# Kernel tuning notes

Measured on AMD Instinct MI355X. Metric: run time of the kernel, lower is better.

## Reference

```python
import jax, jax.numpy as jnp
import numpy as np
from jax import lax


def conv3d(x, w, b):
    # x: [B,C,H,W,D], w: [O,I,kh,kw,kd], SAME padding (matches padding=k//2 for odd k)
    out = lax.conv_general_dilated(
        x, w, window_strides=(1, 1, 1), padding='SAME',
        dimension_numbers=('NCDHW', 'OIDHW', 'NCDHW'))
    return out + b[None, :, None, None, None]


def setup_inputs() -> dict:
    key = jax.random.key(0)
    ks = jax.random.split(key, 9)
    B, C, H, W, D = 2, 64, 16, 16, 16
    P = 64  # pab_channels
    s = 0.05
    return {
        'x': jax.random.normal(ks[0], (B, C, H, W, D), jnp.float32),
        'top_w': jax.random.normal(ks[1], (P, C, 1, 1, 1), jnp.float32) * s,
        'top_b': jax.random.normal(ks[2], (P,), jnp.float32) * s,
        'center_w': jax.random.normal(ks[3], (P, C, 1, 1, 1), jnp.float32) * s,
        'center_b': jax.random.normal(ks[4], (P,), jnp.float32) * s,
        'bottom_w': jax.random.normal(ks[5], (C, C, 3, 3, 3), jnp.float32) * s,
        'bottom_b': jax.random.normal(ks[6], (C,), jnp.float32) * s,
        'out_w': jax.random.normal(ks[7], (C, C, 3, 3, 3), jnp.float32) * s,
        'out_b': jax.random.normal(ks[8], (C,), jnp.float32) * s,
    }


def reference(x, top_w, top_b, center_w, center_b, bottom_w, bottom_b, out_w, out_b):
    B, C, H, W, D = x.shape
    N = H * W * D
    x_top = conv3d(x, top_w, top_b).reshape(B, -1, N)            # [B,P,N]
    x_center = conv3d(x, center_w, center_b).reshape(B, -1, N)   # [B,P,N]
    x_bottom = conv3d(x, bottom_w, bottom_b).reshape(B, C, N)    # [B,C,N]
    # sp_map[b,n,m] = sum_p center[b,p,n] * top[b,p,m]
    sp = jnp.einsum('bpn,bpm->bnm', x_center, x_top)             # [B,N,N]
    # GLOBAL softmax over the entire flattened NxN map per batch element
    sp = jax.nn.softmax(sp.reshape(B, N * N), axis=1).reshape(B, N, N)
    sp = jnp.einsum('bnm,bcm->bnc', sp, x_bottom)                # [B,N,C]
    # faithful to torch: plain reshape [B,N,C] -> [B,C,H,W,D] (no transpose)
    sp = sp.reshape(B, C, H, W, D)
    return conv3d(x + sp, out_w, out_b)
```

## Files before the change

### kernel.cpp

```cpp
#include <hip/hip_runtime.h>


typedef __attribute__((ext_vector_type(8))) short bf16x8;
typedef __attribute__((ext_vector_type(4))) short short4v;
typedef __attribute__((ext_vector_type(4))) float f32x4;

#define DEVI static __device__ __forceinline__

DEVI f32x4 MFMA16(bf16x8 a, bf16x8 b, f32x4 c) {
  return __builtin_amdgcn_mfma_f32_16x16x32_bf16(a, b, c, 0, 0, 0);
}
DEVI f32x4 zero4() { return (f32x4){0.f, 0.f, 0.f, 0.f}; }

DEVI unsigned short f2bf(float f) {
  unsigned u = __float_as_uint(f);
  return (unsigned short)((u + 0x7fffu + ((u >> 16) & 1u)) >> 16);
}
DEVI float bf2f(unsigned short u) { return __uint_as_float((unsigned)u << 16); }
DEVI float fexp2(float x) { return __builtin_amdgcn_exp2f(x); }

DEVI unsigned cvtpk(float lo, float hi) {
  unsigned d;
  asm("v_cvt_pk_bf16_f32 %0, %1, %2" : "=v"(d) : "v"(lo), "v"(hi));
  return d;
}
DEVI bf16x8 pack8(f32x4 a, f32x4 b) {
  union { unsigned u[4]; bf16x8 v; } r;
  r.u[0] = cvtpk(a[0], a[1]);
  r.u[1] = cvtpk(a[2], a[3]);
  r.u[2] = cvtpk(b[0], b[1]);
  r.u[3] = cvtpk(b[2], b[3]);
  return r.v;
}

DEVI void gll16(const unsigned short* g, unsigned short* l) {
  __builtin_amdgcn_global_load_lds(
      (const __attribute__((address_space(1))) void*)g,
      (__attribute__((address_space(3))) void*)l, 16, 0, 0);
}

DEVI int permM(int n) {
  return (n & ~63) | (n & 32) | ((n & 12) << 1) | ((n & 16) >> 2) | (n & 3);
}

__global__ void k_prep(const float* __restrict__ tw, const float* __restrict__ cw,
                       const float* __restrict__ bw, const float* __restrict__ ow,
                       const float* __restrict__ x,
                       unsigned short* __restrict__ wkTopF, unsigned short* __restrict__ wkCenF,
                       unsigned short* __restrict__ wkBotF, unsigned short* __restrict__ wkOutF,
                       unsigned short* __restrict__ xT, unsigned short* __restrict__ zbuf) {
  __shared__ float tile[64][65];
  int bx = blockIdx.x;
  int tid = threadIdx.x;
  if (bx == 0 && tid < 64) zbuf[tid] = 0;
  if (bx < 432) {
    int t = bx * 256 + tid;
    if (t < 4096) {
      int co = t >> 6, ci = t & 63;
      int cog = co >> 4, col = co & 15, kc = ci >> 5, kg = (ci & 31) >> 3, e = ci & 7;
      int dst = (((cog * 2 + kc) * 64) + col + 16 * kg) * 8 + e;
      wkTopF[dst] = f2bf(tw[t]);
      wkCenF[dst] = f2bf(cw[t]);
    }
    int k = t % 27;
    int ci = (t / 27) & 63;
    int co = t / (27 * 64);
    int cog = co >> 4, col = co & 15, kc = ci >> 5, kg = (ci & 31) >> 3, e = ci & 7;
    int dst = ((((cog * 27 + k) * 2 + kc) * 64) + col + 16 * kg) * 8 + e;
    wkBotF[dst] = f2bf(bw[t]);
    wkOutF[dst] = f2bf(ow[t]);
    return;
  }
  int bx2 = bx - 432;
  int b = bx2 >> 6;
  int n0 = (bx2 & 63) << 6;
  {
    int nl = tid & 63, cq = tid >> 6;
    const float* xb = x + (size_t)b * 262144;
#pragma unroll
    for (int j = 0; j < 16; j++) {
      int c = cq * 16 + j;
      tile[c][nl] = xb[(size_t)c * 4096 + n0 + nl];
    }
  }
  __syncthreads();
  {
    int n = tid >> 2, c0 = (tid & 3) << 4;
    bf16x8 o0, o1;
#pragma unroll
    for (int j = 0; j < 8; j++) {
      o0[j] = (short)f2bf(tile[c0 + j][n]);
      o1[j] = (short)f2bf(tile[c0 + 8 + j][n]);
    }
    unsigned short* dst = xT + ((size_t)(b * 4096 + n0 + n)) * 64 + c0;
    *(bf16x8*)(dst) = o0;
    *(bf16x8*)(dst + 8) = o1;
  }
}

template <int OMODE>
DEVI void conv3_body(int bx, int t,
                     const unsigned short* __restrict__ wkF,
                     const unsigned short* __restrict__ xTb,
                     const float* __restrict__ bias,
                     const unsigned short* __restrict__ zbuf,
                     float* __restrict__ outF, unsigned short* __restrict__ outH,
                     unsigned short* hl) {
  int ch = bx & 1, wp = (bx >> 1) & 7, h = (bx >> 4) & 15, b = bx >> 8;
  int lane = t & 63, w = t >> 6;
  int col = lane & 15, kg = lane >> 4;
  const unsigned short* xb = xTb + (size_t)b * 262144;
  int row8 = lane >> 3, blk = lane & 7;
#pragma unroll
  for (int q = 0; q < 6; q++) {
    int vi0 = w * 48 + q * 8;
    int vi = vi0 + row8;
    int dhv = vi >> 6, wv = (vi >> 4) & 3, dv = vi & 15;
    int hh = h + dhv - 1, ww = wp * 2 + wv - 1;
    bool val = ((unsigned)hh < 16u) & ((unsigned)ww < 16u);
    int sw = blk ^ (vi & 7);
    const unsigned short* src =
        val ? (xb + ((size_t)((hh * 256 + ww * 16 + dv)) << 6) + sw * 8) : (zbuf + blk * 8);
    gll16(src, hl + vi0 * 64);
  }
  __syncthreads();
  int wi = w >> 1;
  int cg = ch * 2 + (w & 1);
  const char* hlb = (const char*)hl;
  f32x4 acc0 = zero4(), acc1 = zero4();
#pragma unroll
  for (int k = 0; k < 27; k++) {
    const int dh = k / 9;
    const int dw = (k / 3) % 3;
    const int dz = k % 3 - 1;
    int dsum = col + dz;
    bool vd = (unsigned)dsum < 16u;
    int dcl = vd ? dsum : col;
    int sv = dh * 64 + (wi + dw) * 16 + dcl;
    const unsigned short* wfk = wkF + (((size_t)(cg * 27 + k)) << 10) + lane * 8;
#pragma unroll
    for (int kc = 0; kc < 2; kc++) {
      bf16x8 av = *(const bf16x8*)(wfk + (kc << 9));
      int g = (kc * 4 + kg) ^ (sv & 7);
      bf16x8 bv = *(const bf16x8*)(hlb + sv * 128 + g * 16);
      if (!vd) bv = (bf16x8){0, 0, 0, 0, 0, 0, 0, 0};
      if (kc == 0) acc0 = MFMA16(av, bv, acc0);
      else acc1 = MFMA16(av, bv, acc1);
    }
  }
  int n0c = h * 256 + (wp * 2 + wi) * 16 + col;
  int nst = (OMODE == 2) ? permM(n0c) : n0c;
#pragma unroll
  for (int r = 0; r < 4; r++) {
    int co = ch * 32 + (w & 1) * 16 + kg * 4 + r;
    float v = acc0[r] + acc1[r] + bias[co];
    if (OMODE == 2)
      outH[(size_t)(b * 64 + co) * 4096 + nst] = f2bf(v);
    else
      outF[(size_t)(b * 64 + co) * 4096 + nst] = v;
  }
}

__global__ __launch_bounds__(256, 2) void k_convA(
    const unsigned short* __restrict__ wkTf, const unsigned short* __restrict__ wkCf,
    const unsigned short* __restrict__ wkBf, const unsigned short* __restrict__ xTb,
    const float* __restrict__ tbias, const float* __restrict__ cbias,
    const float* __restrict__ bbias, const unsigned short* __restrict__ zbuf,
    unsigned short* __restrict__ topT, unsigned short* __restrict__ cenT,
    unsigned short* __restrict__ botS) {
  __shared__ __align__(16) unsigned short hl[192 * 64];
  int bx0 = blockIdx.x;
  int t = threadIdx.x;
  if (bx0 >= 512) {
    conv3_body<2>(bx0 - 512, t, wkBf, xTb, bbias, zbuf, nullptr, botS, hl);
    return;
  }
  int lane = t & 63, wid = t >> 6;
  int col = lane & 15, kg = lane >> 4;
  int bx = bx0;
  int b = bx >> 8;
  int rest = bx & 255;
  int nt = rest >> 1, ch = rest & 1;
  int cg = ch * 2 + (wid >> 1);
  int co0 = ch * 32 + (wid >> 1) * 16;
  int n0c = nt * 32 + (wid & 1) * 16 + col;
  const unsigned short* xb = xTb + (size_t)b * 262144;
  f32x4 aT0 = zero4(), aT1 = zero4(), aC0 = zero4(), aC1 = zero4();
#pragma unroll
  for (int kc = 0; kc < 2; kc++) {
    bf16x8 bv = *(const bf16x8*)(xb + (size_t)n0c * 64 + kc * 32 + kg * 8);
    bf16x8 avT = *(const bf16x8*)(wkTf + (((size_t)cg * 2 + kc) * 64 + lane) * 8);
    bf16x8 avC = *(const bf16x8*)(wkCf + (((size_t)cg * 2 + kc) * 64 + lane) * 8);
    if (kc == 0) {
      aT0 = MFMA16(avT, bv, aT0);
      aC0 = MFMA16(avC, bv, aC0);
    } else {
      aT1 = MFMA16(avT, bv, aT1);
      aC1 = MFMA16(avC, bv, aC1);
    }
  }
  const float LOG2E = 1.4426950408889634f;
  short4v sT, sC;
#pragma unroll
  for (int r = 0; r < 4; r++) {
    float bvT = tbias[co0 + kg * 4 + r];
    float bvC = cbias[co0 + kg * 4 + r];
    sT[r] = (short)f2bf(aT0[r] + aT1[r] + bvT);
    sC[r] = (short)f2bf((aC0[r] + aC1[r] + bvC) * LOG2E);
  }
  size_t o = (size_t)(b * 4096 + n0c) * 64 + co0 + kg * 4;
  *(short4v*)(topT + o) = sT;
  *(short4v*)(cenT + o) = sC;
}

__global__ __launch_bounds__(256, 2) void k_convOut(
    const unsigned short* __restrict__ wkOf, const unsigned short* __restrict__ xTb,
    const float* __restrict__ bias, const unsigned short* __restrict__ zbuf,
    float* __restrict__ outF) {
  __shared__ __align__(16) unsigned short hl[192 * 64];
  conv3_body<1>(blockIdx.x, threadIdx.x, wkOf, xTb, bias, zbuf, outF, nullptr, hl);
}

__global__ __launch_bounds__(256, 2) void k_pass2(
    const unsigned short* __restrict__ cenT, const unsigned short* __restrict__ topT,
    const unsigned short* __restrict__ botS,
    unsigned short* __restrict__ part, float* __restrict__ Zpart) {
  __shared__ __align__(16) unsigned short topS[2][4096];
  __shared__ __align__(16) unsigned short botL[2][4096];
  __shared__ float zred[4];
  int bx = blockIdx.x;
  int b = bx >> 8;
  int ntp = (bx >> 3) & 31;
  int mc = bx & 7;
  int t = threadIdx.x;
  int lane = t & 63, w = t >> 6;
  int col = lane & 15, kg = lane >> 4;
  const unsigned short* cb = cenT + (size_t)b * 262144;
  const unsigned short* tb = topT + (size_t)b * 262144;
  const unsigned short* bb = botS + (size_t)b * 262144;
  int nA = ntp * 128 + w * 16;
  int mcBase = mc * 512;
  int row8 = lane >> 3, blk = lane & 7;
  int sw = blk ^ (row8 & 7);

  bf16x8 aA0 = *(const bf16x8*)(cb + (size_t)(nA + col) * 64 + kg * 8);
  bf16x8 aA1 = *(const bf16x8*)(cb + (size_t)(nA + col) * 64 + 32 + kg * 8);
  bf16x8 aB0 = *(const bf16x8*)(cb + (size_t)(nA + 64 + col) * 64 + kg * 8);
  bf16x8 aB1 = *(const bf16x8*)(cb + (size_t)(nA + 64 + col) * 64 + 32 + kg * 8);

  if (w < 2) {
#pragma unroll
    for (int q = 0; q < 4; q++) {
      int s = w * 4 + q;
      gll16(tb + (size_t)(mcBase + s * 8 + row8) * 64 + sw * 8, &topS[0][s * 512]);
    }
  } else {
#pragma unroll
    for (int q = 0; q < 4; q++) {
      int s = (w - 2) * 4 + q;
      gll16(bb + (size_t)(s * 8 + row8) * 4096 + mcBase + sw * 8, &botL[0][s * 512]);
    }
  }
  __syncthreads();

  f32x4 accOA[4], accOB[4];
#pragma unroll
  for (int ct = 0; ct < 4; ct++) {
    accOA[ct] = zero4();
    accOB[ct] = zero4();
  }
  float zs = 0.f;
  int swc = (col & 7) << 3;

  for (int j = 0; j < 8; j++) {
    int cur = j & 1;
    if (j < 7) {
      int m0n = mcBase + (j + 1) * 64;
      if (w < 2) {
#pragma unroll
        for (int q = 0; q < 4; q++) {
          int s = w * 4 + q;
          gll16(tb + (size_t)(m0n + s * 8 + row8) * 64 + sw * 8, &topS[cur ^ 1][s * 512]);
        }
      } else {
#pragma unroll
        for (int q = 0; q < 4; q++) {
          int s = (w - 2) * 4 + q;
          gll16(bb + (size_t)(s * 8 + row8) * 4096 + m0n + sw * 8, &botL[cur ^ 1][s * 512]);
        }
      }
    }
    f32x4 sA[4], sB[4];
#pragma unroll
    for (int mt = 0; mt < 4; mt++) {
      bf16x8 b0 = *(const bf16x8*)&topS[cur][(mt * 16 + col) * 64 + ((kg * 8) ^ swc)];
      bf16x8 b1 = *(const bf16x8*)&topS[cur][(mt * 16 + col) * 64 + ((32 + kg * 8) ^ swc)];
      sA[mt] = MFMA16(b1, aA1, MFMA16(b0, aA0, zero4()));
      sB[mt] = MFMA16(b1, aB1, MFMA16(b0, aB0, zero4()));
    }
#pragma unroll
    for (int mt = 0; mt < 4; mt++)
#pragma unroll
      for (int r = 0; r < 4; r++) {
        sA[mt][r] = fexp2(sA[mt][r]);
        sB[mt][r] = fexp2(sB[mt][r]);
        zs += sA[mt][r] + sB[mt][r];
      }
#pragma unroll
    for (int kc = 0; kc < 2; kc++) {
      bf16x8 paA = pack8(sA[2 * kc], sA[2 * kc + 1]);
      bf16x8 paB = pack8(sB[2 * kc], sB[2 * kc + 1]);
#pragma unroll
      for (int ct = 0; ct < 4; ct++) {
        bf16x8 bv = *(const bf16x8*)&botL[cur][(ct * 16 + col) * 64 + ((kc * 32 + kg * 8) ^ swc)];
        accOA[ct] = MFMA16(paA, bv, accOA[ct]);
        accOB[ct] = MFMA16(paB, bv, accOB[ct]);
      }
    }
    __syncthreads();
  }
  unsigned short* po = part + (((size_t)(b * 8 + mc) * 4096 + nA) << 6);
#pragma unroll
  for (int ct = 0; ct < 4; ct++)
#pragma unroll
    for (int r = 0; r < 4; r++) {
      po[(kg * 4 + r) * 64 + ct * 16 + col] = f2bf(accOA[ct][r]);
      po[(64 + kg * 4 + r) * 64 + ct * 16 + col] = f2bf(accOB[ct][r]);
    }
#pragma unroll
  for (int off = 32; off; off >>= 1) zs += __shfl_xor(zs, off);
  if (lane == 0) zred[w] = zs;
  __syncthreads();
  if (t == 0) Zpart[b * 256 + ntp * 8 + mc] = zred[0] + zred[1] + zred[2] + zred[3];
}

__global__ void k_xt1(const float* __restrict__ x, const unsigned short* __restrict__ part,
                      const float* __restrict__ Zpart, unsigned short* __restrict__ xT) {
  __shared__ float tile[64][65];
  __shared__ float zr[4];
  int bx = blockIdx.x;
  int b = bx >> 6;
  int n0 = (bx & 63) << 6;
  int t = threadIdx.x;
  float zv = Zpart[b * 256 + t];
#pragma unroll
  for (int off = 32; off; off >>= 1) zv += __shfl_xor(zv, off);
  if ((t & 63) == 0) zr[t >> 6] = zv;
  __syncthreads();
  float invZ = 1.0f / (zr[0] + zr[1] + zr[2] + zr[3]);
  {
    int c = t >> 2, nl16 = (t & 3) << 4;
    int nt6 = n0 >> 6;
    float acc[16];
#pragma unroll
    for (int k = 0; k < 16; k++) acc[k] = 0.f;
#pragma unroll
    for (int mcq = 0; mcq < 8; mcq++) {
      const unsigned short* pp =
          part + (((size_t)(b * 8 + mcq) * 4096) + c * 64 + nt6) * 64 + nl16;
      bf16x8 v0 = *(const bf16x8*)pp;
      bf16x8 v1 = *(const bf16x8*)(pp + 8);
#pragma unroll
      for (int k = 0; k < 8; k++) {
        acc[k] += bf2f((unsigned short)v0[k]);
        acc[8 + k] += bf2f((unsigned short)v1[k]);
      }
    }
    const float* xb = x + (size_t)b * 262144 + (size_t)c * 4096 + n0 + nl16;
#pragma unroll
    for (int q = 0; q < 4; q++) {
      f32x4 xv = *(const f32x4*)(xb + q * 4);
#pragma unroll
      for (int k = 0; k < 4; k++) tile[c][nl16 + q * 4 + k] = xv[k] + acc[q * 4 + k] * invZ;
    }
  }
  __syncthreads();
  {
    int n = t >> 2, c0 = (t & 3) << 4;
    bf16x8 o0, o1;
#pragma unroll
    for (int j = 0; j < 8; j++) {
      o0[j] = (short)f2bf(tile[c0 + j][n]);
      o1[j] = (short)f2bf(tile[c0 + 8 + j][n]);
    }
    unsigned short* dst = xT + ((size_t)(b * 4096 + n0 + n)) * 64 + c0;
    *(bf16x8*)(dst) = o0;
    *(bf16x8*)(dst + 8) = o1;
  }
}

extern "C" void kernel_launch(void* const* d_in, const int* in_sizes, int n_in,
                              void* d_out, int out_size, void* d_ws, size_t ws_size,
                              hipStream_t stream) {
  const float* x = (const float*)d_in[0];
  const float* tw = (const float*)d_in[1];
  const float* tb = (const float*)d_in[2];
  const float* cw = (const float*)d_in[3];
  const float* cbb = (const float*)d_in[4];
  const float* bw = (const float*)d_in[5];
  const float* bb = (const float*)d_in[6];
  const float* ow = (const float*)d_in[7];
  const float* ob = (const float*)d_in[8];
  float* out = (float*)d_out;
  char* ws = (char*)d_ws;

  unsigned short* wkTopF = (unsigned short*)(ws + 0);
  unsigned short* wkCenF = (unsigned short*)(ws + 8192);
  unsigned short* wkBotF = (unsigned short*)(ws + 16384);
  unsigned short* wkOutF = (unsigned short*)(ws + 237568);
  unsigned short* xT = (unsigned short*)(ws + 458752);
  unsigned short* topT = (unsigned short*)(ws + 1507328);
  unsigned short* cenT = (unsigned short*)(ws + 2555904);
  unsigned short* botS = (unsigned short*)(ws + 3604480);
  unsigned short* yT = (unsigned short*)(ws + 4653056);
  unsigned short* part = (unsigned short*)(ws + 5701632);
  float* Zpart = (float*)(ws + 14090240);
  unsigned short* zbuf = (unsigned short*)(ws + 14092288);

  k_prep<<<560, 256, 0, stream>>>(tw, cw, bw, ow, x, wkTopF, wkCenF, wkBotF, wkOutF, xT, zbuf);
  k_convA<<<1024, 256, 0, stream>>>(wkTopF, wkCenF, wkBotF, xT, tb, cbb, bb, zbuf, topT, cenT, botS);
  k_pass2<<<512, 256, 0, stream>>>(cenT, topT, botS, part, Zpart);
  k_xt1<<<128, 256, 0, stream>>>(x, part, Zpart, yT);
  k_convOut<<<512, 256, 0, stream>>>(wkOutF, yT, ob, zbuf, out);
}
```

Baseline: 43.95 us.

## Regrid conv3 blocks to cover all channels and widen pass2 to 512 threads

After: 47.87 us. +8.9%, slower.

```diff
diff --git a/kernel.cpp b/kernel.cpp
--- a/kernel.cpp
+++ b/kernel.cpp
@@ -106,7 +106,7 @@
                      const unsigned short* __restrict__ zbuf,
                      float* __restrict__ outF, unsigned short* __restrict__ outH,
                      unsigned short* hl) {
-  int ch = bx & 1, wp = (bx >> 1) & 7, h = (bx >> 4) & 15, b = bx >> 8;
+  int b = bx >> 7, h = (bx >> 3) & 15, wp = bx & 7;
   int lane = t & 63, w = t >> 6;
   int col = lane & 15, kg = lane >> 4;
   const unsigned short* xb = xTb + (size_t)b * 262144;
@@ -124,8 +124,8 @@
     gll16(src, hl + vi0 * 64);
   }
   __syncthreads();
-  int wi = w >> 1;
-  int cg = ch * 2 + (w & 1);
+  int wi = w & 1;
+  int ch = w >> 1;
   const char* hlb = (const char*)hl;
   f32x4 acc0 = zero4(), acc1 = zero4();
 #pragma unroll
@@ -137,27 +137,32 @@
     bool vd = (unsigned)dsum < 16u;
     int dcl = vd ? dsum : col;
     int sv = dh * 64 + (wi + dw) * 16 + dcl;
-    const unsigned short* wfk = wkF + (((size_t)(cg * 27 + k)) << 10) + lane * 8;
+    const unsigned short* wf0 = wkF + (((size_t)((2 * ch) * 27 + k)) << 10) + lane * 8;
+    const unsigned short* wf1 = wkF + (((size_t)((2 * ch + 1) * 27 + k)) << 10) + lane * 8;
 #pragma unroll
     for (int kc = 0; kc < 2; kc++) {
-      bf16x8 av = *(const bf16x8*)(wfk + (kc << 9));
       int g = (kc * 4 + kg) ^ (sv & 7);
       bf16x8 bv = *(const bf16x8*)(hlb + sv * 128 + g * 16);
       if (!vd) bv = (bf16x8){0, 0, 0, 0, 0, 0, 0, 0};
-      if (kc == 0) acc0 = MFMA16(av, bv, acc0);
-      else acc1 = MFMA16(av, bv, acc1);
+      bf16x8 av0 = *(const bf16x8*)(wf0 + (kc << 9));
+      bf16x8 av1 = *(const bf16x8*)(wf1 + (kc << 9));
+      acc0 = MFMA16(av0, bv, acc0);
+      acc1 = MFMA16(av1, bv, acc1);
     }
   }
   int n0c = h * 256 + (wp * 2 + wi) * 16 + col;
   int nst = (OMODE == 2) ? permM(n0c) : n0c;
 #pragma unroll
-  for (int r = 0; r < 4; r++) {
-    int co = ch * 32 + (w & 1) * 16 + kg * 4 + r;
-    float v = acc0[r] + acc1[r] + bias[co];
-    if (OMODE == 2)
-      outH[(size_t)(b * 64 + co) * 4096 + nst] = f2bf(v);
-    else
-      outF[(size_t)(b * 64 + co) * 4096 + nst] = v;
+  for (int cgi = 0; cgi < 2; cgi++) {
+#pragma unroll
+    for (int r = 0; r < 4; r++) {
+      int co = (ch * 2 + cgi) * 16 + kg * 4 + r;
+      float v = (cgi ? acc1[r] : acc0[r]) + bias[co];
+      if (OMODE == 2)
+        outH[(size_t)(b * 64 + co) * 4096 + nst] = f2bf(v);
+      else
+        outF[(size_t)(b * 64 + co) * 4096 + nst] = v;
+    }
   }
 }
 
@@ -221,17 +226,17 @@
   conv3_body<1>(blockIdx.x, threadIdx.x, wkOf, xTb, bias, zbuf, outF, nullptr, hl);
 }
 
-__global__ __launch_bounds__(256, 2) void k_pass2(
+__global__ __launch_bounds__(512, 2) void k_pass2(
     const unsigned short* __restrict__ cenT, const unsigned short* __restrict__ topT,
     const unsigned short* __restrict__ botS,
     unsigned short* __restrict__ part, float* __restrict__ Zpart) {
   __shared__ __align__(16) unsigned short topS[2][4096];
   __shared__ __align__(16) unsigned short botL[2][4096];
-  __shared__ float zred[4];
+  __shared__ float zred[8];
   int bx = blockIdx.x;
-  int b = bx >> 8;
-  int ntp = (bx >> 3) & 31;
-  int mc = bx & 7;
+  int b = bx >> 7;
+  int ntp = (bx >> 2) & 31;
+  int mc = bx & 3;
   int t = threadIdx.x;
   int lane = t & 63, w = t >> 6;
   int col = lane & 15, kg = lane >> 4;
@@ -239,99 +244,93 @@
   const unsigned short* tb = topT + (size_t)b * 262144;
   const unsigned short* bb = botS + (size_t)b * 262144;
   int nA = ntp * 128 + w * 16;
-  int mcBase = mc * 512;
+  int mcBase = mc * 1024;
   int row8 = lane >> 3, blk = lane & 7;
   int sw = blk ^ (row8 & 7);
 
   bf16x8 aA0 = *(const bf16x8*)(cb + (size_t)(nA + col) * 64 + kg * 8);
   bf16x8 aA1 = *(const bf16x8*)(cb + (size_t)(nA + col) * 64 + 32 + kg * 8);
-  bf16x8 aB0 = *(const bf16x8*)(cb + (size_t)(nA + 64 + col) * 64 + kg * 8);
-  bf16x8 aB1 = *(const bf16x8*)(cb + (size_t)(nA + 64 + col) * 64 + 32 + kg * 8);
-
-  if (w < 2) {
-#pragma unroll
-    for (int q = 0; q < 4; q++) {
-      int s = w * 4 + q;
+
+  if (w < 4) {
+#pragma unroll
+    for (int q = 0; q < 2; q++) {
+      int s = w * 2 + q;
       gll16(tb + (size_t)(mcBase + s * 8 + row8) * 64 + sw * 8, &topS[0][s * 512]);
     }
   } else {
 #pragma unroll
-    for (int q = 0; q < 4; q++) {
-      int s = (w - 2) * 4 + q;
+    for (int q = 0; q < 2; q++) {
+      int s = (w - 4) * 2 + q;
       gll16(bb + (size_t)(s * 8 + row8) * 4096 + mcBase + sw * 8, &botL[0][s * 512]);
     }
   }
   __syncthreads();
 
-  f32x4 accOA[4], accOB[4];
-#pragma unroll
-  for (int ct = 0; ct < 4; ct++) {
-    accOA[ct] = zero4();
-    accOB[ct] = zero4();
-  }
+  f32x4 accO[4];
+#pragma unroll
+  for (int ct = 0; ct < 4; ct++) accO[ct] = zero4();
   float zs = 0.f;
   int swc = (col & 7) << 3;
 
-  for (int j = 0; j < 8; j++) {
+  for (int j = 0; j < 16; j++) {
     int cur = j & 1;
-    if (j < 7) {
+    if (j < 15) {
       int m0n = mcBase + (j + 1) * 64;
-      if (w < 2) {
-#pragma unroll
-        for (int q = 0; q < 4; q++) {
-          int s = w * 4 + q;
+      if (w < 4) {
+#pragma unroll
+        for (int q = 0; q < 2; q++) {
+          int s = w * 2 + q;
           gll16(tb + (size_t)(m0n + s * 8 + row8) * 64 + sw * 8, &topS[cur ^ 1][s * 512]);
         }
       } else {
 #pragma unroll
-        for (int q = 0; q < 4; q++) {
-          int s = (w - 2) * 4 + q;
+        for (int q = 0; q < 2; q++) {
+          int s = (w - 4) * 2 + q;
           gll16(bb + (size_t)(s * 8 + row8) * 4096 + m0n + sw * 8, &botL[cur ^ 1][s * 512]);
         }
       }
     }
-    f32x4 sA[4], sB[4];
+    f32x4 sA[4];
 #pragma unroll
     for (int mt = 0; mt < 4; mt++) {
       bf16x8 b0 = *(const bf16x8*)&topS[cur][(mt * 16 + col) * 64 + ((kg * 8) ^ swc)];
       bf16x8 b1 = *(const bf16x8*)&topS[cur][(mt * 16 + col) * 64 + ((32 + kg * 8) ^ swc)];
       sA[mt] = MFMA16(b1, aA1, MFMA16(b0, aA0, zero4()));
-      sB[mt] = MFMA16(b1, aB1, MFMA16(b0, aB0, zero4()));
     }
 #pragma unroll
     for (int mt = 0; mt < 4; mt++)
 #pragma unroll
       for (int r = 0; r < 4; r++) {
         sA[mt][r] = fexp2(sA[mt][r]);
-        sB[mt][r] = fexp2(sB[mt][r]);
-        zs += sA[mt][r] + sB[mt][r];
+        zs += sA[mt][r];
       }
 #pragma unroll
     for (int kc = 0; kc < 2; kc++) {
-      bf16x8 paA = pack8(sA[2 * kc], sA[2 * kc + 1]);
-      bf16x8 paB = pack8(sB[2 * kc], sB[2 * kc + 1]);
+      bf16x8 pa = pack8(sA[2 * kc], sA[2 * kc + 1]);
 #pragma unroll
       for (int ct = 0; ct < 4; ct++) {
         bf16x8 bv = *(const bf16x8*)&botL[cur][(ct * 16 + col) * 64 + ((kc * 32 + kg * 8) ^ swc)];
-        accOA[ct] = MFMA16(paA, bv, accOA[ct]);
-        accOB[ct] = MFMA16(paB, bv, accOB[ct]);
+        accO[ct] = MFMA16(pa, bv, accO[ct]);
       }
     }
     __syncthreads();
   }
-  unsigned short* po = part + (((size_t)(b * 8 + mc) * 4096 + nA) << 6);
+  unsigned short* po = part + (((size_t)(b * 4 + mc) * 4096 + nA) << 6);
 #pragma unroll
   for (int ct = 0; ct < 4; ct++)
 #pragma unroll
-    for (int r = 0; r < 4; r++) {
-      po[(kg * 4 + r) * 64 + ct * 16 + col] = f2bf(accOA[ct][r]);
-      po[(64 + kg * 4 + r) * 64 + ct * 16 + col] = f2bf(accOB[ct][r]);
-    }
+    for (int r = 0; r < 4; r++)
+      po[(kg * 4 + r) * 64 + ct * 16 + col] = f2bf(accO[ct][r]);
 #pragma unroll
   for (int off = 32; off; off >>= 1) zs += __shfl_xor(zs, off);
   if (lane == 0) zred[w] = zs;
   __syncthreads();
-  if (t == 0) Zpart[b * 256 + ntp * 8 + mc] = zred[0] + zred[1] + zred[2] + zred[3];
+  if (t == 0) {
+    float z = 0.f;
+#pragma unroll
+    for (int i = 0; i < 8; i++) z += zred[i];
+    Zpart[b * 128 + ntp * 4 + mc] = z;
+  }
 }
 
 __global__ void k_xt1(const float* __restrict__ x, const unsigned short* __restrict__ part,
@@ -342,12 +341,12 @@
   int b = bx >> 6;
   int n0 = (bx & 63) << 6;
   int t = threadIdx.x;
-  float zv = Zpart[b * 256 + t];
+  float zv = (t < 128) ? Zpart[b * 128 + t] : 0.f;
 #pragma unroll
   for (int off = 32; off; off >>= 1) zv += __shfl_xor(zv, off);
   if ((t & 63) == 0) zr[t >> 6] = zv;
   __syncthreads();
-  float invZ = 1.0f / (zr[0] + zr[1] + zr[2] + zr[3]);
+  float invZ = 1.0f / (zr[0] + zr[1]);
   {
     int c = t >> 2, nl16 = (t & 3) << 4;
     int nt6 = n0 >> 6;
@@ -355,9 +354,9 @@
 #pragma unroll
     for (int k = 0; k < 16; k++) acc[k] = 0.f;
 #pragma unroll
-    for (int mcq = 0; mcq < 8; mcq++) {
+    for (int mcq = 0; mcq < 4; mcq++) {
       const unsigned short* pp =
-          part + (((size_t)(b * 8 + mcq) * 4096) + c * 64 + nt6) * 64 + nl16;
+          part + (((size_t)(b * 4 + mcq) * 4096) + c * 64 + nt6) * 64 + nl16;
       bf16x8 v0 = *(const bf16x8*)pp;
       bf16x8 v1 = *(const bf16x8*)(pp + 8);
 #pragma unroll
@@ -418,8 +417,8 @@
   unsigned short* zbuf = (unsigned short*)(ws + 14092288);
 
   k_prep<<<560, 256, 0, stream>>>(tw, cw, bw, ow, x, wkTopF, wkCenF, wkBotF, wkOutF, xT, zbuf);
-  k_convA<<<1024, 256, 0, stream>>>(wkTopF, wkCenF, wkBotF, xT, tb, cbb, bb, zbuf, topT, cenT, botS);
-  k_pass2<<<512, 256, 0, stream>>>(cenT, topT, botS, part, Zpart);
+  k_convA<<<768, 256, 0, stream>>>(wkTopF, wkCenF, wkBotF, xT, tb, cbb, bb, zbuf, topT, cenT, botS);
+  k_pass2<<<256, 512, 0, stream>>>(cenT, topT, botS, part, Zpart);
   k_xt1<<<128, 256, 0, stream>>>(x, part, Zpart, yT);
-  k_convOut<<<512, 256, 0, stream>>>(wkOutF, yT, ob, zbuf, out);
-}
+  k_convOut<<<256, 256, 0, stream>>>(wkOutF, yT, ob, zbuf, out);
+}
```
